# Kernel tuning notes

Measured on AMD Instinct MI355X. Metric: run time of the kernel, lower is better.

## Reference

```python
import jax, jax.numpy as jnp
import numpy as np

B, C, H, W = 16, 128, 32, 32
CHOICES, OUT_C, OH, OW = 4, 128, 32, 32
INIT_WEIGHTS = [0.25, 0.25, 0.25, 0.25]
INIT_STD = 0.01


def setup_inputs() -> dict:
    key = jax.random.key(0)
    ks = jax.random.split(key, 6)
    x = jax.random.normal(ks[0], (B, C, H, W), dtype=jnp.float32)
    # 1x1 conv1d weights == dense matrices [out, in]; xavier-normal-ish scale
    Wq = jax.random.normal(ks[1], (C, C), dtype=jnp.float32) * (1.0 / np.sqrt(C))
    Wk = jax.random.normal(ks[2], (C, C), dtype=jnp.float32) * (1.0 / np.sqrt(C))
    Wv = jax.random.normal(ks[3], (CHOICES * OUT_C, C), dtype=jnp.float32) * (1.0 / np.sqrt(C))
    gamma = jnp.ones((1,), dtype=jnp.float32)  # learnable scalar (0 at init; use 1 to exercise math)
    # mask init: per-choice mean = init_weights[i] * out_choices, std = init_std
    means = jnp.asarray([w * CHOICES for w in INIT_WEIGHTS], dtype=jnp.float32)
    mask = jax.random.normal(ks[4], (1, OUT_C, OH, OW, CHOICES), dtype=jnp.float32) * INIT_STD + means
    return {"x": x, "Wq": Wq, "Wk": Wk, "Wv": Wv, "gamma": gamma, "mask": mask}


def reference(x, Wq, Wk, Wv, gamma, mask):
    b, c, h, w = x.shape
    n = h * w
    x2 = x.reshape(b, c, n)                                   # [b, C, N]
    f = jnp.einsum('oc,bcn->bon', Wq, x2)                     # query  [b, C, N]
    g = jnp.einsum('oc,bcn->bon', Wk, x2)                     # key    [b, C, N]
    hv = jnp.einsum('oc,bcn->bon', Wv, x2)                    # value  [b, CHOICES*OUT_C, N]
    # beta = softmax(f^T g) over dim 1 (rows), per torch code
    scores = jnp.einsum('bcn,bcm->bnm', f, g)                 # [b, N, N]
    beta = jax.nn.softmax(scores, axis=1)
    out = gamma * jnp.einsum('bkn,bnm->bkm', hv, beta)        # [b, CHOICES*OUT_C, N]
    out = out.reshape(b, CHOICES, OUT_C, OH, OW)              # no resize: H==OH, W==OW
    out = jnp.transpose(out, (0, 2, 3, 4, 1))                 # [b, OUT_C, OH, OW, CHOICES]
    return out + mask
```

## Files before the change

kernel.cpp:

```cpp
#include <hip/hip_runtime.h>

#define B 16
#define C 128
#define NN 1024
#define KV 512
#define CHO 4

typedef _Float16 f16x8 __attribute__((ext_vector_type(8)));
typedef float f32x4 __attribute__((ext_vector_type(4)));

__device__ __forceinline__ unsigned short f2h(float v) {
  _Float16 h = (_Float16)v;
  return __builtin_bit_cast(unsigned short, h);
}
__device__ __forceinline__ unsigned int packh2(float a, float b) {
  return (unsigned int)f2h(a) | ((unsigned int)f2h(b) << 16);
}
__device__ __forceinline__ f16x8 ldcvt8(const float* __restrict__ p) {
  float4 a = *reinterpret_cast<const float4*>(p);
  float4 b = *reinterpret_cast<const float4*>(p + 4);
  f16x8 r;
  r[0] = (_Float16)a.x; r[1] = (_Float16)a.y; r[2] = (_Float16)a.z; r[3] = (_Float16)a.w;
  r[4] = (_Float16)b.x; r[5] = (_Float16)b.y; r[6] = (_Float16)b.z; r[7] = (_Float16)b.w;
  return r;
}

__global__ __launch_bounds__(256, 4) void proj_kernel(
    const float* __restrict__ x, const float* __restrict__ Wq,
    const float* __restrict__ Wk, const float* __restrict__ Wv,
    unsigned short* __restrict__ fT, unsigned short* __restrict__ gT,
    unsigned short* __restrict__ hv)
{
  int wg = blockIdx.x;
  wg = (wg & 7) * 384 + (wg >> 3);
  const int b   = wg / 192;
  const int rem = wg % 192;
  const int rt  = rem % 12;
  const int n0  = (rem / 12) * 64;

  __shared__ __align__(16) unsigned short XT[64][136];

  const int t = threadIdx.x;
  const int w = t >> 6, l = t & 63, lg = l >> 4, lm = l & 15;

  {
    const float* xb = x + (size_t)b * C * NN;
    #pragma unroll
    for (int i = 0; i < 8; ++i) {
      int flat = t + i * 256;
      int c  = flat >> 4;
      int ng = flat & 15;
      float4 v = *reinterpret_cast<const float4*>(xb + (size_t)c * NN + n0 + ng * 4);
      XT[ng * 4 + 0][c] = f2h(v.x);
      XT[ng * 4 + 1][c] = f2h(v.y);
      XT[ng * 4 + 2][c] = f2h(v.z);
      XT[ng * 4 + 3][c] = f2h(v.w);
    }
  }
  __syncthreads();

  if (rt < 4) {
    const float* Wsrc = (rt < 2) ? Wq : Wk;
    unsigned short* dst = (rt < 2) ? fT : gT;
    const int c0 = (rt & 1) * 64;
    const int r  = c0 + 16 * w + lm;
    f16x8 af[4];
    #pragma unroll
    for (int c4 = 0; c4 < 4; ++c4)
      af[c4] = ldcvt8(Wsrc + (size_t)r * C + c4 * 32 + lg * 8);
    #pragma unroll
    for (int nt4 = 0; nt4 < 4; ++nt4) {
      f32x4 acc = {0.f, 0.f, 0.f, 0.f};
      #pragma unroll
      for (int c4 = 0; c4 < 4; ++c4) {
        f16x8 xb = *reinterpret_cast<const f16x8*>(&XT[16 * nt4 + lm][c4 * 32 + lg * 8]);
        acc = __builtin_amdgcn_mfma_f32_16x16x32_f16(af[c4], xb, acc, 0, 0, 0);
      }
      int n = n0 + 16 * nt4 + lm;
      ushort4 o = { f2h(acc[0]), f2h(acc[1]), f2h(acc[2]), f2h(acc[3]) };
      *reinterpret_cast<ushort4*>(dst + ((size_t)(b * NN) + n) * C + c0 + 16 * w + 4 * lg) = o;
    }
  } else {
    const int kk = (rt - 4) * 64 + 16 * w + lm;
    f16x8 wb[4];
    #pragma unroll
    for (int c4 = 0; c4 < 4; ++c4)
      wb[c4] = ldcvt8(Wv + (size_t)kk * C + c4 * 32 + lg * 8);
    #pragma unroll
    for (int nt4 = 0; nt4 < 4; ++nt4) {
      f32x4 acc = {0.f, 0.f, 0.f, 0.f};
      #pragma unroll
      for (int c4 = 0; c4 < 4; ++c4) {
        f16x8 xa = *reinterpret_cast<const f16x8*>(&XT[16 * nt4 + lm][c4 * 32 + lg * 8]);
        acc = __builtin_amdgcn_mfma_f32_16x16x32_f16(xa, wb[c4], acc, 0, 0, 0);
      }
      ushort4 o = { f2h(acc[0]), f2h(acc[1]), f2h(acc[2]), f2h(acc[3]) };
      *reinterpret_cast<ushort4*>(hv + ((size_t)(b * KV) + kk) * NN + n0 + 16 * nt4 + 4 * lg) = o;
    }
  }
}

__global__ __launch_bounds__(256, 1) void attn_kernel(
    const unsigned short* __restrict__ fT, const unsigned short* __restrict__ gT,
    const unsigned short* __restrict__ hv, const float* __restrict__ gamma,
    const float* __restrict__ mask, float* __restrict__ out)
{
  int wg = blockIdx.x;
  wg = (wg & 7) * 32 + (wg >> 3);
  const int b  = wg >> 4;
  const int m0 = (wg & 15) * 64;

  const int t = threadIdx.x;
  const int w = t >> 6, l = t & 63, lg = l >> 4, lm = l & 15;

  __shared__ __align__(16) unsigned short P_lds[2][64][72];
  __shared__ float resc_s[2][64];
  __shared__ float lsum_s[64];

  f16x8 qf[4];
  {
    const unsigned short* qp = gT + ((size_t)(b * NN) + m0 + 16 * w + lm) * C + lg * 8;
    #pragma unroll
    for (int c4 = 0; c4 < 4; ++c4)
      qf[c4] = *reinterpret_cast<const f16x8*>(qp + c4 * 32);
  }

  f32x4 acc[8][4];
  #pragma unroll
  for (int kt = 0; kt < 8; ++kt)
    #pragma unroll
    for (int mt = 0; mt < 4; ++mt)
      acc[kt][mt] = (f32x4){0.f, 0.f, 0.f, 0.f};

  float M = -3.0e38f, Lpart = 0.f;

  const unsigned short* kp = fT + ((size_t)(b * NN) + lm) * C + lg * 8;
  const unsigned short* vp = hv + ((size_t)(b * KV) + 128 * w + lm) * NN + lg * 8;

  #pragma unroll 1
  for (int it = 0; it < 16; ++it) {
    const int n0  = it * 64;
    const int cur = it & 1;

    f16x8 vf[8][2];
    #pragma unroll
    for (int kt = 0; kt < 8; ++kt) {
      vf[kt][0] = *reinterpret_cast<const f16x8*>(vp + (size_t)(16 * kt) * NN + n0);
      vf[kt][1] = *reinterpret_cast<const f16x8*>(vp + (size_t)(16 * kt) * NN + n0 + 32);
    }

    f32x4 st[4];
    #pragma unroll
    for (int j = 0; j < 4; ++j) st[j] = (f32x4){0.f, 0.f, 0.f, 0.f};
    #pragma unroll
    for (int c4 = 0; c4 < 4; ++c4) {
      #pragma unroll
      for (int j = 0; j < 4; ++j) {
        f16x8 kf = *reinterpret_cast<const f16x8*>(kp + (size_t)(n0 + 16 * j) * C + c4 * 32);
        st[j] = __builtin_amdgcn_mfma_f32_16x16x32_f16(kf, qf[c4], st[j], 0, 0, 0);
      }
    }

    float cmax = -3.0e38f;
    #pragma unroll
    for (int j = 0; j < 4; ++j)
      cmax = fmaxf(cmax, fmaxf(fmaxf(st[j][0], st[j][1]), fmaxf(st[j][2], st[j][3])));
    cmax = fmaxf(cmax, __shfl_xor(cmax, 16, 64));
    cmax = fmaxf(cmax, __shfl_xor(cmax, 32, 64));
    float r = 1.0f;
    if (!__all(cmax <= M + 8.0f)) {
      float newM = fmaxf(M, cmax);
      r = __expf(M - newM);
      M = newM;
      Lpart *= r;
    }
    float p[16];
    float ls = 0.f;
    #pragma unroll
    for (int j = 0; j < 4; ++j) {
      p[4 * j + 0] = __expf(st[j][0] - M);
      p[4 * j + 1] = __expf(st[j][1] - M);
      p[4 * j + 2] = __expf(st[j][2] - M);
      p[4 * j + 3] = __expf(st[j][3] - M);
      ls += (p[4 * j] + p[4 * j + 1]) + (p[4 * j + 2] + p[4 * j + 3]);
    }
    Lpart += ls;
    if (lg == 0) resc_s[cur][16 * w + lm] = r;
    {
      unsigned short* prow = &P_lds[cur][16 * w + lm][0];
      #pragma unroll
      for (int j = 0; j < 4; ++j) {
        *(unsigned int*)(prow + 16 * j + 4 * lg)     = packh2(p[4 * j],     p[4 * j + 1]);
        *(unsigned int*)(prow + 16 * j + 4 * lg + 2) = packh2(p[4 * j + 2], p[4 * j + 3]);
      }
    }
    __syncthreads();

    float rr0 = resc_s[cur][lm],      rr1 = resc_s[cur][16 + lm],
          rr2 = resc_s[cur][32 + lm], rr3 = resc_s[cur][48 + lm];
    if (!__all((rr0 == 1.f) & (rr1 == 1.f) & (rr2 == 1.f) & (rr3 == 1.f))) {
      #pragma unroll
      for (int kt = 0; kt < 8; ++kt) {
        acc[kt][0] *= rr0; acc[kt][1] *= rr1;
        acc[kt][2] *= rr2; acc[kt][3] *= rr3;
      }
    }

    f16x8 pt[4][2];
    #pragma unroll
    for (int mt = 0; mt < 4; ++mt) {
      pt[mt][0] = *reinterpret_cast<const f16x8*>(&P_lds[cur][16 * mt + lm][8 * lg]);
      pt[mt][1] = *reinterpret_cast<const f16x8*>(&P_lds[cur][16 * mt + lm][32 + 8 * lg]);
    }

    #pragma unroll
    for (int kt = 0; kt < 8; ++kt) {
      #pragma unroll
      for (int mt = 0; mt < 4; ++mt) {
        acc[kt][mt] = __builtin_amdgcn_mfma_f32_16x16x32_f16(vf[kt][0], pt[mt][0], acc[kt][mt], 0, 0, 0);
        acc[kt][mt] = __builtin_amdgcn_mfma_f32_16x16x32_f16(vf[kt][1], pt[mt][1], acc[kt][mt], 0, 0, 0);
      }
    }
  }

  float Lp = Lpart;
  Lp += __shfl_xor(Lp, 16, 64);
  Lp += __shfl_xor(Lp, 32, 64);
  __syncthreads();
  if (lg == 0) lsum_s[16 * w + lm] = Lp;
  __syncthreads();

  const float gam = gamma[0];
  float scv[4] = { gam / lsum_s[lm],      gam / lsum_s[16 + lm],
                   gam / lsum_s[32 + lm], gam / lsum_s[48 + lm] };

  #pragma unroll
  for (int kt = 0; kt < 8; ++kt) {
    #pragma unroll
    for (int mt = 0; mt < 4; ++mt) {
      int m = m0 + 16 * mt + lm;
      #pragma unroll
      for (int reg = 0; reg < 4; ++reg) {
        int oc = 16 * kt + 4 * lg + reg;
        float v = acc[kt][mt][reg] * scv[mt] + mask[((size_t)oc * NN + m) * CHO + w];
        out[(((size_t)(b * 128 + oc)) * NN + m) * CHO + w] = v;
      }
    }
  }
}

extern "C" void kernel_launch(void* const* d_in, const int* in_sizes, int n_in,
                              void* d_out, int out_size, void* d_ws, size_t ws_size,
                              hipStream_t stream) {
  const float* x     = (const float*)d_in[0];
  const float* Wq    = (const float*)d_in[1];
  const float* Wk    = (const float*)d_in[2];
  const float* Wv    = (const float*)d_in[3];
  const float* gamma = (const float*)d_in[4];
  const float* mask  = (const float*)d_in[5];
  float* out = (float*)d_out;

  unsigned short* fT = (unsigned short*)d_ws;
  unsigned short* gT = fT + (size_t)B * NN * C;
  unsigned short* hv = gT + (size_t)B * NN * C;

  proj_kernel<<<dim3(3072), 256, 0, stream>>>(x, Wq, Wk, Wv, fT, gT, hv);
  attn_kernel<<<dim3(256), 256, 0, stream>>>(fT, gT, hv, gamma, mask, out);
}
```

Before: 103.5 us.

## Split attention workgroup into 8 waves with specialized score and value roles

The attention kernel now runs 512 threads per workgroup. Four waves compute scores and softmax plus 48 value rows each, and the other four waves handle only value rows, 80 each, which gives more wave-level parallelism and cuts accumulator registers per wave. V fragments for the next tile are prefetched after the PV step so global load latency overlaps the next iteration. The uneven split (3 vs 5 k-tiles) tries to balance softmax work against MFMA work, but it adds divergence between wave groups and a block-wide barrier on every iteration.

After: 133.5 us. 28.9% more time.

```diff
diff --git a/kernel.cpp b/kernel.cpp
--- a/kernel.cpp
+++ b/kernel.cpp
@@ -23,6 +23,9 @@
   r[0] = (_Float16)a.x; r[1] = (_Float16)a.y; r[2] = (_Float16)a.z; r[3] = (_Float16)a.w;
   r[4] = (_Float16)b.x; r[5] = (_Float16)b.y; r[6] = (_Float16)b.z; r[7] = (_Float16)b.w;
   return r;
+}
+__device__ __forceinline__ f32x4 MFMA(f16x8 a, f16x8 b, f32x4 c) {
+  return __builtin_amdgcn_mfma_f32_16x16x32_f16(a, b, c, 0, 0, 0);
 }
 
 __global__ __launch_bounds__(256, 4) void proj_kernel(
@@ -74,7 +77,7 @@
       #pragma unroll
       for (int c4 = 0; c4 < 4; ++c4) {
         f16x8 xb = *reinterpret_cast<const f16x8*>(&XT[16 * nt4 + lm][c4 * 32 + lg * 8]);
-        acc = __builtin_amdgcn_mfma_f32_16x16x32_f16(af[c4], xb, acc, 0, 0, 0);
+        acc = MFMA(af[c4], xb, acc);
       }
       int n = n0 + 16 * nt4 + lm;
       ushort4 o = { f2h(acc[0]), f2h(acc[1]), f2h(acc[2]), f2h(acc[3]) };
@@ -92,7 +95,7 @@
       #pragma unroll
       for (int c4 = 0; c4 < 4; ++c4) {
         f16x8 xa = *reinterpret_cast<const f16x8*>(&XT[16 * nt4 + lm][c4 * 32 + lg * 8]);
-        acc = __builtin_amdgcn_mfma_f32_16x16x32_f16(xa, wb[c4], acc, 0, 0, 0);
+        acc = MFMA(xa, wb[c4], acc);
       }
       ushort4 o = { f2h(acc[0]), f2h(acc[1]), f2h(acc[2]), f2h(acc[3]) };
       *reinterpret_cast<ushort4*>(hv + ((size_t)(b * KV) + kk) * NN + n0 + 16 * nt4 + 4 * lg) = o;
@@ -100,7 +103,55 @@
   }
 }
 
-__global__ __launch_bounds__(256, 1) void attn_kernel(
+template<int NKT>
+__device__ __forceinline__ void rescale_acc(f32x4 (&acc)[5][4],
+    float rr0, float rr1, float rr2, float rr3) {
+  #pragma unroll
+  for (int kt = 0; kt < NKT; ++kt) {
+    acc[kt][0] *= rr0; acc[kt][1] *= rr1;
+    acc[kt][2] *= rr2; acc[kt][3] *= rr3;
+  }
+}
+template<int NKT>
+__device__ __forceinline__ void pv_step(f32x4 (&acc)[5][4], const f16x8 (&vf)[5][2],
+                                        const f16x8 (&pt)[4][2]) {
+  #pragma unroll
+  for (int kt = 0; kt < NKT; ++kt)
+    #pragma unroll
+    for (int mt = 0; mt < 4; ++mt) {
+      acc[kt][mt] = MFMA(vf[kt][0], pt[mt][0], acc[kt][mt]);
+      acc[kt][mt] = MFMA(vf[kt][1], pt[mt][1], acc[kt][mt]);
+    }
+}
+template<int NKT>
+__device__ __forceinline__ void vf_load(f16x8 (&vf)[5][2],
+    const unsigned short* __restrict__ vp, int n0) {
+  #pragma unroll
+  for (int kt = 0; kt < NKT; ++kt) {
+    vf[kt][0] = *reinterpret_cast<const f16x8*>(vp + (size_t)(16 * kt) * NN + n0);
+    vf[kt][1] = *reinterpret_cast<const f16x8*>(vp + (size_t)(16 * kt) * NN + n0 + 32);
+  }
+}
+template<int NKT>
+__device__ __forceinline__ void store_out(const f32x4 (&acc)[5][4],
+    const float* __restrict__ mask, float* __restrict__ out,
+    const float (&scv)[4], int b, int m0, int lg, int lm, int kbase) {
+  #pragma unroll
+  for (int kt = 0; kt < NKT; ++kt)
+    #pragma unroll
+    for (int mt = 0; mt < 4; ++mt) {
+      int m = m0 + 16 * mt + lm;
+      #pragma unroll
+      for (int reg = 0; reg < 4; ++reg) {
+        int k  = kbase + 16 * kt + 4 * lg + reg;
+        int oc = k & 127, ch = k >> 7;
+        float v = acc[kt][mt][reg] * scv[mt] + mask[((size_t)oc * NN + m) * CHO + ch];
+        out[(((size_t)(b * 128 + oc)) * NN + m) * CHO + ch] = v;
+      }
+    }
+}
+
+__global__ __launch_bounds__(512, 1) void attn_kernel(
     const unsigned short* __restrict__ fT, const unsigned short* __restrict__ gT,
     const unsigned short* __restrict__ hv, const float* __restrict__ gamma,
     const float* __restrict__ mask, float* __restrict__ out)
@@ -112,22 +163,23 @@
 
   const int t = threadIdx.x;
   const int w = t >> 6, l = t & 63, lg = l >> 4, lm = l & 15;
+  const int kbase = (w < 4) ? 48 * w : 192 + 80 * (w - 4);
 
   __shared__ __align__(16) unsigned short P_lds[2][64][72];
   __shared__ float resc_s[2][64];
   __shared__ float lsum_s[64];
 
   f16x8 qf[4];
-  {
+  if (w < 4) {
     const unsigned short* qp = gT + ((size_t)(b * NN) + m0 + 16 * w + lm) * C + lg * 8;
     #pragma unroll
     for (int c4 = 0; c4 < 4; ++c4)
       qf[c4] = *reinterpret_cast<const f16x8*>(qp + c4 * 32);
   }
 
-  f32x4 acc[8][4];
-  #pragma unroll
-  for (int kt = 0; kt < 8; ++kt)
+  f32x4 acc[5][4];
+  #pragma unroll
+  for (int kt = 0; kt < 5; ++kt)
     #pragma unroll
     for (int mt = 0; mt < 4; ++mt)
       acc[kt][mt] = (f32x4){0.f, 0.f, 0.f, 0.f};
@@ -135,91 +187,81 @@
   float M = -3.0e38f, Lpart = 0.f;
 
   const unsigned short* kp = fT + ((size_t)(b * NN) + lm) * C + lg * 8;
-  const unsigned short* vp = hv + ((size_t)(b * KV) + 128 * w + lm) * NN + lg * 8;
+  const unsigned short* vp = hv + ((size_t)(b * KV) + kbase + lm) * NN + lg * 8;
+
+  f16x8 vf[5][2];
+  if (w < 4) vf_load<3>(vf, vp, 0); else vf_load<5>(vf, vp, 0);
 
   #pragma unroll 1
   for (int it = 0; it < 16; ++it) {
     const int n0  = it * 64;
     const int cur = it & 1;
-
-    f16x8 vf[8][2];
-    #pragma unroll
-    for (int kt = 0; kt < 8; ++kt) {
-      vf[kt][0] = *reinterpret_cast<const f16x8*>(vp + (size_t)(16 * kt) * NN + n0);
-      vf[kt][1] = *reinterpret_cast<const f16x8*>(vp + (size_t)(16 * kt) * NN + n0 + 32);
-    }
-
-    f32x4 st[4];
-    #pragma unroll
-    for (int j = 0; j < 4; ++j) st[j] = (f32x4){0.f, 0.f, 0.f, 0.f};
-    #pragma unroll
-    for (int c4 = 0; c4 < 4; ++c4) {
+    const int nx0 = ((it + 1) & 15) * 64;
+
+    if (w < 4) {
+      f32x4 st[4];
+      #pragma unroll
+      for (int j = 0; j < 4; ++j) st[j] = (f32x4){0.f, 0.f, 0.f, 0.f};
+      #pragma unroll
+      for (int c4 = 0; c4 < 4; ++c4) {
+        #pragma unroll
+        for (int j = 0; j < 4; ++j) {
+          f16x8 kf = *reinterpret_cast<const f16x8*>(kp + (size_t)(n0 + 16 * j) * C + c4 * 32);
+          st[j] = MFMA(kf, qf[c4], st[j]);
+        }
+      }
+
+      float cmax = -3.0e38f;
+      #pragma unroll
+      for (int j = 0; j < 4; ++j)
+        cmax = fmaxf(cmax, fmaxf(fmaxf(st[j][0], st[j][1]), fmaxf(st[j][2], st[j][3])));
+      cmax = fmaxf(cmax, __shfl_xor(cmax, 16, 64));
+      cmax = fmaxf(cmax, __shfl_xor(cmax, 32, 64));
+      float r = 1.0f;
+      if (!__all(cmax <= M + 8.0f)) {
+        float newM = fmaxf(M, cmax);
+        r = __expf(M - newM);
+        M = newM;
+        Lpart *= r;
+      }
+      float ls = 0.f;
       #pragma unroll
       for (int j = 0; j < 4; ++j) {
-        f16x8 kf = *reinterpret_cast<const f16x8*>(kp + (size_t)(n0 + 16 * j) * C + c4 * 32);
-        st[j] = __builtin_amdgcn_mfma_f32_16x16x32_f16(kf, qf[c4], st[j], 0, 0, 0);
-      }
-    }
-
-    float cmax = -3.0e38f;
-    #pragma unroll
-    for (int j = 0; j < 4; ++j)
-      cmax = fmaxf(cmax, fmaxf(fmaxf(st[j][0], st[j][1]), fmaxf(st[j][2], st[j][3])));
-    cmax = fmaxf(cmax, __shfl_xor(cmax, 16, 64));
-    cmax = fmaxf(cmax, __shfl_xor(cmax, 32, 64));
-    float r = 1.0f;
-    if (!__all(cmax <= M + 8.0f)) {
-      float newM = fmaxf(M, cmax);
-      r = __expf(M - newM);
-      M = newM;
-      Lpart *= r;
-    }
-    float p[16];
-    float ls = 0.f;
-    #pragma unroll
-    for (int j = 0; j < 4; ++j) {
-      p[4 * j + 0] = __expf(st[j][0] - M);
-      p[4 * j + 1] = __expf(st[j][1] - M);
-      p[4 * j + 2] = __expf(st[j][2] - M);
-      p[4 * j + 3] = __expf(st[j][3] - M);
-      ls += (p[4 * j] + p[4 * j + 1]) + (p[4 * j + 2] + p[4 * j + 3]);
-    }
-    Lpart += ls;
-    if (lg == 0) resc_s[cur][16 * w + lm] = r;
-    {
+        st[j][0] = __expf(st[j][0] - M);
+        st[j][1] = __expf(st[j][1] - M);
+        st[j][2] = __expf(st[j][2] - M);
+        st[j][3] = __expf(st[j][3] - M);
+        ls += (st[j][0] + st[j][1]) + (st[j][2] + st[j][3]);
+      }
+      Lpart += ls;
+      if (lg == 0) resc_s[cur][16 * w + lm] = r;
       unsigned short* prow = &P_lds[cur][16 * w + lm][0];
       #pragma unroll
       for (int j = 0; j < 4; ++j) {
-        *(unsigned int*)(prow + 16 * j + 4 * lg)     = packh2(p[4 * j],     p[4 * j + 1]);
-        *(unsigned int*)(prow + 16 * j + 4 * lg + 2) = packh2(p[4 * j + 2], p[4 * j + 3]);
+        *(unsigned int*)(prow + 16 * j + 4 * lg)     = packh2(st[j][0], st[j][1]);
+        *(unsigned int*)(prow + 16 * j + 4 * lg + 2) = packh2(st[j][2], st[j][3]);
       }
     }
     __syncthreads();
 
     float rr0 = resc_s[cur][lm],      rr1 = resc_s[cur][16 + lm],
           rr2 = resc_s[cur][32 + lm], rr3 = resc_s[cur][48 + lm];
-    if (!__all((rr0 == 1.f) & (rr1 == 1.f) & (rr2 == 1.f) & (rr3 == 1.f))) {
-      #pragma unroll
-      for (int kt = 0; kt < 8; ++kt) {
-        acc[kt][0] *= rr0; acc[kt][1] *= rr1;
-        acc[kt][2] *= rr2; acc[kt][3] *= rr3;
-      }
-    }
-
     f16x8 pt[4][2];
     #pragma unroll
     for (int mt = 0; mt < 4; ++mt) {
       pt[mt][0] = *reinterpret_cast<const f16x8*>(&P_lds[cur][16 * mt + lm][8 * lg]);
       pt[mt][1] = *reinterpret_cast<const f16x8*>(&P_lds[cur][16 * mt + lm][32 + 8 * lg]);
     }
-
-    #pragma unroll
-    for (int kt = 0; kt < 8; ++kt) {
-      #pragma unroll
-      for (int mt = 0; mt < 4; ++mt) {
-        acc[kt][mt] = __builtin_amdgcn_mfma_f32_16x16x32_f16(vf[kt][0], pt[mt][0], acc[kt][mt], 0, 0, 0);
-        acc[kt][mt] = __builtin_amdgcn_mfma_f32_16x16x32_f16(vf[kt][1], pt[mt][1], acc[kt][mt], 0, 0, 0);
-      }
+    bool needr = !__all((rr0 == 1.f) & (rr1 == 1.f) & (rr2 == 1.f) & (rr3 == 1.f));
+
+    if (w < 4) {
+      if (needr) rescale_acc<3>(acc, rr0, rr1, rr2, rr3);
+      pv_step<3>(acc, vf, pt);
+      vf_load<3>(vf, vp, nx0);
+    } else {
+      if (needr) rescale_acc<5>(acc, rr0, rr1, rr2, rr3);
+      pv_step<5>(acc, vf, pt);
+      vf_load<5>(vf, vp, nx0);
     }
   }
 
@@ -227,26 +269,15 @@
   Lp += __shfl_xor(Lp, 16, 64);
   Lp += __shfl_xor(Lp, 32, 64);
   __syncthreads();
-  if (lg == 0) lsum_s[16 * w + lm] = Lp;
+  if (w < 4 && lg == 0) lsum_s[16 * w + lm] = Lp;
   __syncthreads();
 
   const float gam = gamma[0];
   float scv[4] = { gam / lsum_s[lm],      gam / lsum_s[16 + lm],
                    gam / lsum_s[32 + lm], gam / lsum_s[48 + lm] };
 
-  #pragma unroll
-  for (int kt = 0; kt < 8; ++kt) {
-    #pragma unroll
-    for (int mt = 0; mt < 4; ++mt) {
-      int m = m0 + 16 * mt + lm;
-      #pragma unroll
-      for (int reg = 0; reg < 4; ++reg) {
-        int oc = 16 * kt + 4 * lg + reg;
-        float v = acc[kt][mt][reg] * scv[mt] + mask[((size_t)oc * NN + m) * CHO + w];
-        out[(((size_t)(b * 128 + oc)) * NN + m) * CHO + w] = v;
-      }
-    }
-  }
+  if (w < 4) store_out<3>(acc, mask, out, scv, b, m0, lg, lm, kbase);
+  else       store_out<5>(acc, mask, out, scv, b, m0, lg, lm, kbase);
 }
 
 extern "C" void kernel_launch(void* const* d_in, const int* in_sizes, int n_in,
@@ -265,5 +296,5 @@
   unsigned short* hv = gT + (size_t)B * NN * C;
 
   proj_kernel<<<dim3(3072), 256, 0, stream>>>(x, Wq, Wk, Wv, fT, gT, hv);
-  attn_kernel<<<dim3(256), 256, 0, stream>>>(fT, gT, hv, gamma, mask, out);
-}
+  attn_kernel<<<dim3(256), 512, 0, stream>>>(fT, gT, hv, gamma, mask, out);
+}
```

## Split attention key range across two wave groups and merge partial softmax results

Applied to the files above, without the earlier changes.

The attention kernel now runs 512 threads per block: two groups of four waves each process half of the key dimension with their own online-softmax state and their own LDS buffers. The partial results are merged through shared max/sum values. Group 1 writes its scaled partial output to global memory, and group 0 then reads it back and adds its own part plus the mask. V-fragment loads are also moved after the softmax and split into halves to reduce register pressure. The goal is more waves per CU to hide latency, at the cost of an extra global write/read round trip of the output and a block-wide sync.

New measurement: 126.0 us. 1.22x slower.

```diff
diff --git a/kernel.cpp b/kernel.cpp
--- a/kernel.cpp
+++ b/kernel.cpp
@@ -23,6 +23,9 @@
   r[0] = (_Float16)a.x; r[1] = (_Float16)a.y; r[2] = (_Float16)a.z; r[3] = (_Float16)a.w;
   r[4] = (_Float16)b.x; r[5] = (_Float16)b.y; r[6] = (_Float16)b.z; r[7] = (_Float16)b.w;
   return r;
+}
+__device__ __forceinline__ f32x4 MFMA(f16x8 a, f16x8 b, f32x4 c) {
+  return __builtin_amdgcn_mfma_f32_16x16x32_f16(a, b, c, 0, 0, 0);
 }
 
 __global__ __launch_bounds__(256, 4) void proj_kernel(
@@ -74,7 +77,7 @@
       #pragma unroll
       for (int c4 = 0; c4 < 4; ++c4) {
         f16x8 xb = *reinterpret_cast<const f16x8*>(&XT[16 * nt4 + lm][c4 * 32 + lg * 8]);
-        acc = __builtin_amdgcn_mfma_f32_16x16x32_f16(af[c4], xb, acc, 0, 0, 0);
+        acc = MFMA(af[c4], xb, acc);
       }
       int n = n0 + 16 * nt4 + lm;
       ushort4 o = { f2h(acc[0]), f2h(acc[1]), f2h(acc[2]), f2h(acc[3]) };
@@ -92,7 +95,7 @@
       #pragma unroll
       for (int c4 = 0; c4 < 4; ++c4) {
         f16x8 xa = *reinterpret_cast<const f16x8*>(&XT[16 * nt4 + lm][c4 * 32 + lg * 8]);
-        acc = __builtin_amdgcn_mfma_f32_16x16x32_f16(xa, wb[c4], acc, 0, 0, 0);
+        acc = MFMA(xa, wb[c4], acc);
       }
       ushort4 o = { f2h(acc[0]), f2h(acc[1]), f2h(acc[2]), f2h(acc[3]) };
       *reinterpret_cast<ushort4*>(hv + ((size_t)(b * KV) + kk) * NN + n0 + 16 * nt4 + 4 * lg) = o;
@@ -100,7 +103,7 @@
   }
 }
 
-__global__ __launch_bounds__(256, 1) void attn_kernel(
+__global__ __launch_bounds__(512, 2) void attn_kernel(
     const unsigned short* __restrict__ fT, const unsigned short* __restrict__ gT,
     const unsigned short* __restrict__ hv, const float* __restrict__ gamma,
     const float* __restrict__ mask, float* __restrict__ out)
@@ -112,14 +115,16 @@
 
   const int t = threadIdx.x;
   const int w = t >> 6, l = t & 63, lg = l >> 4, lm = l & 15;
-
-  __shared__ __align__(16) unsigned short P_lds[2][64][72];
-  __shared__ float resc_s[2][64];
-  __shared__ float lsum_s[64];
+  const int g = w >> 2, wl = w & 3;
+
+  __shared__ __align__(16) unsigned short P_lds[2][2][64][72];
+  __shared__ float resc_s[2][2][64];
+  __shared__ float gM[2][64];
+  __shared__ float gL[2][64];
 
   f16x8 qf[4];
   {
-    const unsigned short* qp = gT + ((size_t)(b * NN) + m0 + 16 * w + lm) * C + lg * 8;
+    const unsigned short* qp = gT + ((size_t)(b * NN) + m0 + 16 * wl + lm) * C + lg * 8;
     #pragma unroll
     for (int c4 = 0; c4 < 4; ++c4)
       qf[c4] = *reinterpret_cast<const f16x8*>(qp + c4 * 32);
@@ -135,19 +140,13 @@
   float M = -3.0e38f, Lpart = 0.f;
 
   const unsigned short* kp = fT + ((size_t)(b * NN) + lm) * C + lg * 8;
-  const unsigned short* vp = hv + ((size_t)(b * KV) + 128 * w + lm) * NN + lg * 8;
+  const unsigned short* vp = hv + ((size_t)(b * KV) + 128 * wl + lm) * NN + lg * 8;
+  const int nbase = g * 512;
 
   #pragma unroll 1
-  for (int it = 0; it < 16; ++it) {
-    const int n0  = it * 64;
+  for (int it = 0; it < 8; ++it) {
+    const int n0  = nbase + it * 64;
     const int cur = it & 1;
-
-    f16x8 vf[8][2];
-    #pragma unroll
-    for (int kt = 0; kt < 8; ++kt) {
-      vf[kt][0] = *reinterpret_cast<const f16x8*>(vp + (size_t)(16 * kt) * NN + n0);
-      vf[kt][1] = *reinterpret_cast<const f16x8*>(vp + (size_t)(16 * kt) * NN + n0 + 32);
-    }
 
     f32x4 st[4];
     #pragma unroll
@@ -157,7 +156,7 @@
       #pragma unroll
       for (int j = 0; j < 4; ++j) {
         f16x8 kf = *reinterpret_cast<const f16x8*>(kp + (size_t)(n0 + 16 * j) * C + c4 * 32);
-        st[j] = __builtin_amdgcn_mfma_f32_16x16x32_f16(kf, qf[c4], st[j], 0, 0, 0);
+        st[j] = MFMA(kf, qf[c4], st[j]);
       }
     }
 
@@ -174,30 +173,29 @@
       M = newM;
       Lpart *= r;
     }
-    float p[16];
     float ls = 0.f;
     #pragma unroll
     for (int j = 0; j < 4; ++j) {
-      p[4 * j + 0] = __expf(st[j][0] - M);
-      p[4 * j + 1] = __expf(st[j][1] - M);
-      p[4 * j + 2] = __expf(st[j][2] - M);
-      p[4 * j + 3] = __expf(st[j][3] - M);
-      ls += (p[4 * j] + p[4 * j + 1]) + (p[4 * j + 2] + p[4 * j + 3]);
+      st[j][0] = __expf(st[j][0] - M);
+      st[j][1] = __expf(st[j][1] - M);
+      st[j][2] = __expf(st[j][2] - M);
+      st[j][3] = __expf(st[j][3] - M);
+      ls += (st[j][0] + st[j][1]) + (st[j][2] + st[j][3]);
     }
     Lpart += ls;
-    if (lg == 0) resc_s[cur][16 * w + lm] = r;
+    if (lg == 0) resc_s[g][cur][16 * wl + lm] = r;
     {
-      unsigned short* prow = &P_lds[cur][16 * w + lm][0];
+      unsigned short* prow = &P_lds[g][cur][16 * wl + lm][0];
       #pragma unroll
       for (int j = 0; j < 4; ++j) {
-        *(unsigned int*)(prow + 16 * j + 4 * lg)     = packh2(p[4 * j],     p[4 * j + 1]);
-        *(unsigned int*)(prow + 16 * j + 4 * lg + 2) = packh2(p[4 * j + 2], p[4 * j + 3]);
+        *(unsigned int*)(prow + 16 * j + 4 * lg)     = packh2(st[j][0], st[j][1]);
+        *(unsigned int*)(prow + 16 * j + 4 * lg + 2) = packh2(st[j][2], st[j][3]);
       }
     }
     __syncthreads();
 
-    float rr0 = resc_s[cur][lm],      rr1 = resc_s[cur][16 + lm],
-          rr2 = resc_s[cur][32 + lm], rr3 = resc_s[cur][48 + lm];
+    float rr0 = resc_s[g][cur][lm],      rr1 = resc_s[g][cur][16 + lm],
+          rr2 = resc_s[g][cur][32 + lm], rr3 = resc_s[g][cur][48 + lm];
     if (!__all((rr0 == 1.f) & (rr1 == 1.f) & (rr2 == 1.f) & (rr3 == 1.f))) {
       #pragma unroll
       for (int kt = 0; kt < 8; ++kt) {
@@ -206,20 +204,29 @@
       }
     }
 
-    f16x8 pt[4][2];
-    #pragma unroll
-    for (int mt = 0; mt < 4; ++mt) {
-      pt[mt][0] = *reinterpret_cast<const f16x8*>(&P_lds[cur][16 * mt + lm][8 * lg]);
-      pt[mt][1] = *reinterpret_cast<const f16x8*>(&P_lds[cur][16 * mt + lm][32 + 8 * lg]);
-    }
-
-    #pragma unroll
-    for (int kt = 0; kt < 8; ++kt) {
+    #pragma unroll
+    for (int h = 0; h < 2; ++h) {
+      f16x8 vfh[4];
+      #pragma unroll
+      for (int kt = 0; kt < 4; ++kt)
+        vfh[kt] = *reinterpret_cast<const f16x8*>(vp + (size_t)(16 * (4 * h + kt)) * NN + n0);
+      f16x8 vfh2[4];
+      #pragma unroll
+      for (int kt = 0; kt < 4; ++kt)
+        vfh2[kt] = *reinterpret_cast<const f16x8*>(vp + (size_t)(16 * (4 * h + kt)) * NN + n0 + 32);
+      f16x8 pth[4][2];
       #pragma unroll
       for (int mt = 0; mt < 4; ++mt) {
-        acc[kt][mt] = __builtin_amdgcn_mfma_f32_16x16x32_f16(vf[kt][0], pt[mt][0], acc[kt][mt], 0, 0, 0);
-        acc[kt][mt] = __builtin_amdgcn_mfma_f32_16x16x32_f16(vf[kt][1], pt[mt][1], acc[kt][mt], 0, 0, 0);
-      }
+        pth[mt][0] = *reinterpret_cast<const f16x8*>(&P_lds[g][cur][16 * mt + lm][8 * lg]);
+        pth[mt][1] = *reinterpret_cast<const f16x8*>(&P_lds[g][cur][16 * mt + lm][32 + 8 * lg]);
+      }
+      #pragma unroll
+      for (int kt = 0; kt < 4; ++kt)
+        #pragma unroll
+        for (int mt = 0; mt < 4; ++mt) {
+          acc[4 * h + kt][mt] = MFMA(vfh[kt],  pth[mt][0], acc[4 * h + kt][mt]);
+          acc[4 * h + kt][mt] = MFMA(vfh2[kt], pth[mt][1], acc[4 * h + kt][mt]);
+        }
     }
   }
 
@@ -227,25 +234,52 @@
   Lp += __shfl_xor(Lp, 16, 64);
   Lp += __shfl_xor(Lp, 32, 64);
   __syncthreads();
-  if (lg == 0) lsum_s[16 * w + lm] = Lp;
+  if (lg == 0) { gM[g][16 * wl + lm] = M; gL[g][16 * wl + lm] = Lp; }
   __syncthreads();
 
   const float gam = gamma[0];
-  float scv[4] = { gam / lsum_s[lm],      gam / lsum_s[16 + lm],
-                   gam / lsum_s[32 + lm], gam / lsum_s[48 + lm] };
-
+  float sc[4];
   #pragma unroll
-  for (int kt = 0; kt < 8; ++kt) {
-    #pragma unroll
-    for (int mt = 0; mt < 4; ++mt) {
-      int m = m0 + 16 * mt + lm;
-      #pragma unroll
-      for (int reg = 0; reg < 4; ++reg) {
-        int oc = 16 * kt + 4 * lg + reg;
-        float v = acc[kt][mt][reg] * scv[mt] + mask[((size_t)oc * NN + m) * CHO + w];
-        out[(((size_t)(b * 128 + oc)) * NN + m) * CHO + w] = v;
-      }
-    }
+  for (int mt = 0; mt < 4; ++mt) {
+    int mloc = 16 * mt + lm;
+    float M0 = gM[0][mloc], M1 = gM[1][mloc];
+    float L0 = gL[0][mloc], L1 = gL[1][mloc];
+    float Mx = fmaxf(M0, M1);
+    float e0 = __expf(M0 - Mx), e1 = __expf(M1 - Mx);
+    float D  = L0 * e0 + L1 * e1;
+    sc[mt] = gam * ((g == 0) ? e0 : e1) / D;
+  }
+
+  if (g == 1) {
+    #pragma unroll
+    for (int kt = 0; kt < 8; ++kt)
+      #pragma unroll
+      for (int mt = 0; mt < 4; ++mt) {
+        int m = m0 + 16 * mt + lm;
+        #pragma unroll
+        for (int reg = 0; reg < 4; ++reg) {
+          int k  = 128 * wl + 16 * kt + 4 * lg + reg;
+          int oc = k & 127, ch = k >> 7;
+          out[(((size_t)(b * 128 + oc)) * NN + m) * CHO + ch] = acc[kt][mt][reg] * sc[mt];
+        }
+      }
+  }
+  __syncthreads();
+  if (g == 0) {
+    #pragma unroll
+    for (int kt = 0; kt < 8; ++kt)
+      #pragma unroll
+      for (int mt = 0; mt < 4; ++mt) {
+        int m = m0 + 16 * mt + lm;
+        #pragma unroll
+        for (int reg = 0; reg < 4; ++reg) {
+          int k  = 128 * wl + 16 * kt + 4 * lg + reg;
+          int oc = k & 127, ch = k >> 7;
+          size_t oidx = (((size_t)(b * 128 + oc)) * NN + m) * CHO + ch;
+          out[oidx] = out[oidx] + acc[kt][mt][reg] * sc[mt]
+                    + mask[((size_t)oc * NN + m) * CHO + ch];
+        }
+      }
   }
 }
 
@@ -265,5 +299,5 @@
   unsigned short* hv = gT + (size_t)B * NN * C;
 
   proj_kernel<<<dim3(3072), 256, 0, stream>>>(x, Wq, Wk, Wv, fT, gT, hv);
-  attn_kernel<<<dim3(256), 256, 0, stream>>>(fT, gT, hv, gamma, mask, out);
-}
+  attn_kernel<<<dim3(256), 512, 0, stream>>>(fT, gT, hv, gamma, mask, out);
+}
```

## Software-pipeline attention loop: prefetch K/V into registers and overlap scores with PV

Applied to the files above, without the earlier changes.

Restructures the attention main loop into a software pipeline. Each step does the PV MFMAs for tile i while computing the score/softmax for tile i+1 and prefetching K two tiles ahead and V one tile ahead into double-buffered registers. It also moves the P tile through LDS with a single barrier per step. The aim is to hide global-load latency and let score/exp work overlap with the heavy PV MFMAs at one workgroup per CU. The cost is a large rise in register pressure (extra K and V fragment buffers alongside 128 accumulator registers), which risks spills.

Measured after the change: 112.5 us. 1.09x slower.

```diff
diff --git a/kernel.cpp b/kernel.cpp
--- a/kernel.cpp
+++ b/kernel.cpp
@@ -23,6 +23,9 @@
   r[0] = (_Float16)a.x; r[1] = (_Float16)a.y; r[2] = (_Float16)a.z; r[3] = (_Float16)a.w;
   r[4] = (_Float16)b.x; r[5] = (_Float16)b.y; r[6] = (_Float16)b.z; r[7] = (_Float16)b.w;
   return r;
+}
+__device__ __forceinline__ f32x4 MFMA(f16x8 a, f16x8 b, f32x4 c) {
+  return __builtin_amdgcn_mfma_f32_16x16x32_f16(a, b, c, 0, 0, 0);
 }
 
 __global__ __launch_bounds__(256, 4) void proj_kernel(
@@ -74,7 +77,7 @@
       #pragma unroll
       for (int c4 = 0; c4 < 4; ++c4) {
         f16x8 xb = *reinterpret_cast<const f16x8*>(&XT[16 * nt4 + lm][c4 * 32 + lg * 8]);
-        acc = __builtin_amdgcn_mfma_f32_16x16x32_f16(af[c4], xb, acc, 0, 0, 0);
+        acc = MFMA(af[c4], xb, acc);
       }
       int n = n0 + 16 * nt4 + lm;
       ushort4 o = { f2h(acc[0]), f2h(acc[1]), f2h(acc[2]), f2h(acc[3]) };
@@ -92,7 +95,7 @@
       #pragma unroll
       for (int c4 = 0; c4 < 4; ++c4) {
         f16x8 xa = *reinterpret_cast<const f16x8*>(&XT[16 * nt4 + lm][c4 * 32 + lg * 8]);
-        acc = __builtin_amdgcn_mfma_f32_16x16x32_f16(xa, wb[c4], acc, 0, 0, 0);
+        acc = MFMA(xa, wb[c4], acc);
       }
       ushort4 o = { f2h(acc[0]), f2h(acc[1]), f2h(acc[2]), f2h(acc[3]) };
       *reinterpret_cast<ushort4*>(hv + ((size_t)(b * KV) + kk) * NN + n0 + 16 * nt4 + 4 * lg) = o;
@@ -100,65 +103,66 @@
   }
 }
 
-__global__ __launch_bounds__(256, 1) void attn_kernel(
-    const unsigned short* __restrict__ fT, const unsigned short* __restrict__ gT,
-    const unsigned short* __restrict__ hv, const float* __restrict__ gamma,
-    const float* __restrict__ mask, float* __restrict__ out)
+template<int CUR, bool LAST>
+__device__ __forceinline__ void attn_body(
+    int it, f32x4 (&acc)[8][4], const f16x8 (&qf)[4], f16x8 (&kf)[4][4],
+    f16x8 (&vfT)[8][2], f16x8 (&vfO)[8][2],
+    unsigned short (&P_lds)[2][64][72], float (&resc_s)[2][64],
+    const unsigned short* __restrict__ kp, const unsigned short* __restrict__ vp,
+    float& M, float& Lpart, int w, int lg, int lm)
 {
-  int wg = blockIdx.x;
-  wg = (wg & 7) * 32 + (wg >> 3);
-  const int b  = wg >> 4;
-  const int m0 = (wg & 15) * 64;
-
-  const int t = threadIdx.x;
-  const int w = t >> 6, l = t & 63, lg = l >> 4, lm = l & 15;
-
-  __shared__ __align__(16) unsigned short P_lds[2][64][72];
-  __shared__ float resc_s[2][64];
-  __shared__ float lsum_s[64];
-
-  f16x8 qf[4];
-  {
-    const unsigned short* qp = gT + ((size_t)(b * NN) + m0 + 16 * w + lm) * C + lg * 8;
-    #pragma unroll
-    for (int c4 = 0; c4 < 4; ++c4)
-      qf[c4] = *reinterpret_cast<const f16x8*>(qp + c4 * 32);
-  }
-
-  f32x4 acc[8][4];
+  constexpr int NXT = CUR ^ 1;
+
+  f16x8 pt[4][2];
+  #pragma unroll
+  for (int mt = 0; mt < 4; ++mt) {
+    pt[mt][0] = *reinterpret_cast<const f16x8*>(&P_lds[CUR][16 * mt + lm][8 * lg]);
+    pt[mt][1] = *reinterpret_cast<const f16x8*>(&P_lds[CUR][16 * mt + lm][32 + 8 * lg]);
+  }
+  float rr0 = resc_s[CUR][lm],      rr1 = resc_s[CUR][16 + lm],
+        rr2 = resc_s[CUR][32 + lm], rr3 = resc_s[CUR][48 + lm];
+  if (!__all((rr0 == 1.f) & (rr1 == 1.f) & (rr2 == 1.f) & (rr3 == 1.f))) {
+    #pragma unroll
+    for (int kt = 0; kt < 8; ++kt) {
+      acc[kt][0] *= rr0; acc[kt][1] *= rr1;
+      acc[kt][2] *= rr2; acc[kt][3] *= rr3;
+    }
+  }
+
+  if (!LAST) {
+    const int nv = ((it + 1) & 15) * 64;
+    #pragma unroll
+    for (int kt = 0; kt < 8; ++kt) {
+      vfO[kt][0] = *reinterpret_cast<const f16x8*>(vp + (size_t)(16 * kt) * NN + nv);
+      vfO[kt][1] = *reinterpret_cast<const f16x8*>(vp + (size_t)(16 * kt) * NN + nv + 32);
+    }
+  }
+
   #pragma unroll
   for (int kt = 0; kt < 8; ++kt)
     #pragma unroll
-    for (int mt = 0; mt < 4; ++mt)
-      acc[kt][mt] = (f32x4){0.f, 0.f, 0.f, 0.f};
-
-  float M = -3.0e38f, Lpart = 0.f;
-
-  const unsigned short* kp = fT + ((size_t)(b * NN) + lm) * C + lg * 8;
-  const unsigned short* vp = hv + ((size_t)(b * KV) + 128 * w + lm) * NN + lg * 8;
-
-  #pragma unroll 1
-  for (int it = 0; it < 16; ++it) {
-    const int n0  = it * 64;
-    const int cur = it & 1;
-
-    f16x8 vf[8][2];
-    #pragma unroll
-    for (int kt = 0; kt < 8; ++kt) {
-      vf[kt][0] = *reinterpret_cast<const f16x8*>(vp + (size_t)(16 * kt) * NN + n0);
-      vf[kt][1] = *reinterpret_cast<const f16x8*>(vp + (size_t)(16 * kt) * NN + n0 + 32);
-    }
-
+    for (int mt = 0; mt < 4; ++mt) {
+      acc[kt][mt] = MFMA(vfT[kt][0], pt[mt][0], acc[kt][mt]);
+      acc[kt][mt] = MFMA(vfT[kt][1], pt[mt][1], acc[kt][mt]);
+    }
+
+  if (!LAST) {
     f32x4 st[4];
     #pragma unroll
     for (int j = 0; j < 4; ++j) st[j] = (f32x4){0.f, 0.f, 0.f, 0.f};
     #pragma unroll
-    for (int c4 = 0; c4 < 4; ++c4) {
-      #pragma unroll
-      for (int j = 0; j < 4; ++j) {
-        f16x8 kf = *reinterpret_cast<const f16x8*>(kp + (size_t)(n0 + 16 * j) * C + c4 * 32);
-        st[j] = __builtin_amdgcn_mfma_f32_16x16x32_f16(kf, qf[c4], st[j], 0, 0, 0);
-      }
+    for (int c4 = 0; c4 < 4; ++c4)
+      #pragma unroll
+      for (int j = 0; j < 4; ++j)
+        st[j] = MFMA(kf[j][c4], qf[c4], st[j]);
+
+    {
+      const int nk = ((it + 2) & 15) * 64;
+      #pragma unroll
+      for (int j = 0; j < 4; ++j)
+        #pragma unroll
+        for (int c4 = 0; c4 < 4; ++c4)
+          kf[j][c4] = *reinterpret_cast<const f16x8*>(kp + (size_t)(nk + 16 * j) * C + c4 * 32);
     }
 
     float cmax = -3.0e38f;
@@ -174,59 +178,134 @@
       M = newM;
       Lpart *= r;
     }
-    float p[16];
     float ls = 0.f;
     #pragma unroll
     for (int j = 0; j < 4; ++j) {
-      p[4 * j + 0] = __expf(st[j][0] - M);
-      p[4 * j + 1] = __expf(st[j][1] - M);
-      p[4 * j + 2] = __expf(st[j][2] - M);
-      p[4 * j + 3] = __expf(st[j][3] - M);
-      ls += (p[4 * j] + p[4 * j + 1]) + (p[4 * j + 2] + p[4 * j + 3]);
+      st[j][0] = __expf(st[j][0] - M);
+      st[j][1] = __expf(st[j][1] - M);
+      st[j][2] = __expf(st[j][2] - M);
+      st[j][3] = __expf(st[j][3] - M);
+      ls += (st[j][0] + st[j][1]) + (st[j][2] + st[j][3]);
     }
     Lpart += ls;
-    if (lg == 0) resc_s[cur][16 * w + lm] = r;
-    {
-      unsigned short* prow = &P_lds[cur][16 * w + lm][0];
-      #pragma unroll
-      for (int j = 0; j < 4; ++j) {
-        *(unsigned int*)(prow + 16 * j + 4 * lg)     = packh2(p[4 * j],     p[4 * j + 1]);
-        *(unsigned int*)(prow + 16 * j + 4 * lg + 2) = packh2(p[4 * j + 2], p[4 * j + 3]);
-      }
-    }
-    __syncthreads();
-
-    float rr0 = resc_s[cur][lm],      rr1 = resc_s[cur][16 + lm],
-          rr2 = resc_s[cur][32 + lm], rr3 = resc_s[cur][48 + lm];
-    if (!__all((rr0 == 1.f) & (rr1 == 1.f) & (rr2 == 1.f) & (rr3 == 1.f))) {
-      #pragma unroll
-      for (int kt = 0; kt < 8; ++kt) {
-        acc[kt][0] *= rr0; acc[kt][1] *= rr1;
-        acc[kt][2] *= rr2; acc[kt][3] *= rr3;
-      }
-    }
-
-    f16x8 pt[4][2];
-    #pragma unroll
-    for (int mt = 0; mt < 4; ++mt) {
-      pt[mt][0] = *reinterpret_cast<const f16x8*>(&P_lds[cur][16 * mt + lm][8 * lg]);
-      pt[mt][1] = *reinterpret_cast<const f16x8*>(&P_lds[cur][16 * mt + lm][32 + 8 * lg]);
-    }
-
-    #pragma unroll
-    for (int kt = 0; kt < 8; ++kt) {
-      #pragma unroll
-      for (int mt = 0; mt < 4; ++mt) {
-        acc[kt][mt] = __builtin_amdgcn_mfma_f32_16x16x32_f16(vf[kt][0], pt[mt][0], acc[kt][mt], 0, 0, 0);
-        acc[kt][mt] = __builtin_amdgcn_mfma_f32_16x16x32_f16(vf[kt][1], pt[mt][1], acc[kt][mt], 0, 0, 0);
-      }
-    }
-  }
+    if (lg == 0) resc_s[NXT][16 * w + lm] = r;
+    unsigned short* prow = &P_lds[NXT][16 * w + lm][0];
+    #pragma unroll
+    for (int j = 0; j < 4; ++j) {
+      *(unsigned int*)(prow + 16 * j + 4 * lg)     = packh2(st[j][0], st[j][1]);
+      *(unsigned int*)(prow + 16 * j + 4 * lg + 2) = packh2(st[j][2], st[j][3]);
+    }
+  }
+  __syncthreads();
+}
+
+__global__ __launch_bounds__(256, 1) void attn_kernel(
+    const unsigned short* __restrict__ fT, const unsigned short* __restrict__ gT,
+    const unsigned short* __restrict__ hv, const float* __restrict__ gamma,
+    const float* __restrict__ mask, float* __restrict__ out)
+{
+  int wg = blockIdx.x;
+  wg = (wg & 7) * 32 + (wg >> 3);
+  const int b  = wg >> 4;
+  const int m0 = (wg & 15) * 64;
+
+  const int t = threadIdx.x;
+  const int w = t >> 6, l = t & 63, lg = l >> 4, lm = l & 15;
+
+  __shared__ __align__(16) unsigned short P_lds[2][64][72];
+  __shared__ float resc_s[2][64];
+  __shared__ float lsum_s[64];
+
+  f16x8 qf[4];
+  {
+    const unsigned short* qp = gT + ((size_t)(b * NN) + m0 + 16 * w + lm) * C + lg * 8;
+    #pragma unroll
+    for (int c4 = 0; c4 < 4; ++c4)
+      qf[c4] = *reinterpret_cast<const f16x8*>(qp + c4 * 32);
+  }
+
+  f32x4 acc[8][4];
+  #pragma unroll
+  for (int kt = 0; kt < 8; ++kt)
+    #pragma unroll
+    for (int mt = 0; mt < 4; ++mt)
+      acc[kt][mt] = (f32x4){0.f, 0.f, 0.f, 0.f};
+
+  float M = -3.0e38f, Lpart = 0.f;
+
+  const unsigned short* kp = fT + ((size_t)(b * NN) + lm) * C + lg * 8;
+  const unsigned short* vp = hv + ((size_t)(b * KV) + 128 * w + lm) * NN + lg * 8;
+
+  f16x8 kf[4][4];
+  f16x8 vfA[8][2], vfB[8][2];
+
+  #pragma unroll
+  for (int j = 0; j < 4; ++j)
+    #pragma unroll
+    for (int c4 = 0; c4 < 4; ++c4)
+      kf[j][c4] = *reinterpret_cast<const f16x8*>(kp + (size_t)(16 * j) * C + c4 * 32);
+  #pragma unroll
+  for (int kt = 0; kt < 8; ++kt) {
+    vfA[kt][0] = *reinterpret_cast<const f16x8*>(vp + (size_t)(16 * kt) * NN);
+    vfA[kt][1] = *reinterpret_cast<const f16x8*>(vp + (size_t)(16 * kt) * NN + 32);
+  }
+  {
+    f32x4 st[4];
+    #pragma unroll
+    for (int j = 0; j < 4; ++j) st[j] = (f32x4){0.f, 0.f, 0.f, 0.f};
+    #pragma unroll
+    for (int c4 = 0; c4 < 4; ++c4)
+      #pragma unroll
+      for (int j = 0; j < 4; ++j)
+        st[j] = MFMA(kf[j][c4], qf[c4], st[j]);
+
+    #pragma unroll
+    for (int j = 0; j < 4; ++j)
+      #pragma unroll
+      for (int c4 = 0; c4 < 4; ++c4)
+        kf[j][c4] = *reinterpret_cast<const f16x8*>(kp + (size_t)(64 + 16 * j) * C + c4 * 32);
+
+    float cmax = -3.0e38f;
+    #pragma unroll
+    for (int j = 0; j < 4; ++j)
+      cmax = fmaxf(cmax, fmaxf(fmaxf(st[j][0], st[j][1]), fmaxf(st[j][2], st[j][3])));
+    cmax = fmaxf(cmax, __shfl_xor(cmax, 16, 64));
+    cmax = fmaxf(cmax, __shfl_xor(cmax, 32, 64));
+    float newM = fmaxf(M, cmax);
+    float r = __expf(M - newM);
+    M = newM;
+    Lpart *= r;
+    float ls = 0.f;
+    #pragma unroll
+    for (int j = 0; j < 4; ++j) {
+      st[j][0] = __expf(st[j][0] - M);
+      st[j][1] = __expf(st[j][1] - M);
+      st[j][2] = __expf(st[j][2] - M);
+      st[j][3] = __expf(st[j][3] - M);
+      ls += (st[j][0] + st[j][1]) + (st[j][2] + st[j][3]);
+    }
+    Lpart += ls;
+    if (lg == 0) resc_s[0][16 * w + lm] = r;
+    unsigned short* prow = &P_lds[0][16 * w + lm][0];
+    #pragma unroll
+    for (int j = 0; j < 4; ++j) {
+      *(unsigned int*)(prow + 16 * j + 4 * lg)     = packh2(st[j][0], st[j][1]);
+      *(unsigned int*)(prow + 16 * j + 4 * lg + 2) = packh2(st[j][2], st[j][3]);
+    }
+  }
+  __syncthreads();
+
+  #pragma unroll 1
+  for (int it2 = 0; it2 < 7; ++it2) {
+    attn_body<0, false>(2 * it2,     acc, qf, kf, vfA, vfB, P_lds, resc_s, kp, vp, M, Lpart, w, lg, lm);
+    attn_body<1, false>(2 * it2 + 1, acc, qf, kf, vfB, vfA, P_lds, resc_s, kp, vp, M, Lpart, w, lg, lm);
+  }
+  attn_body<0, false>(14, acc, qf, kf, vfA, vfB, P_lds, resc_s, kp, vp, M, Lpart, w, lg, lm);
+  attn_body<1, true >(15, acc, qf, kf, vfB, vfA, P_lds, resc_s, kp, vp, M, Lpart, w, lg, lm);
 
   float Lp = Lpart;
   Lp += __shfl_xor(Lp, 16, 64);
   Lp += __shfl_xor(Lp, 32, 64);
-  __syncthreads();
   if (lg == 0) lsum_s[16 * w + lm] = Lp;
   __syncthreads();
 
```
